# Kernel optimization log

Measured on AMD Instinct MI355X. Metric: run time of the kernel, lower is better.

The kernel has to match this reference:

```python
import jax, jax.numpy as jnp
import numpy as np

B, S, D, H = 4, 2048, 1024, 16
HD = D // H


def setup_inputs() -> dict:
    key = jax.random.key(0)
    k1, k2, k3 = jax.random.split(key, 3)
    x = jax.random.normal(k1, (B, S, D), dtype=jnp.float32)
    # xavier-ish scaling for stable softmax
    W_attn = jax.random.normal(k2, (3 * D, D), dtype=jnp.float32) * (1.0 / np.sqrt(2 * D))
    b_attn = jnp.zeros((3 * D,), dtype=jnp.float32)
    W_out = jax.random.normal(k3, (D, D), dtype=jnp.float32) * (1.0 / np.sqrt(D))
    b_out = jnp.zeros((D,), dtype=jnp.float32)
    return {"x": x, "W_attn": W_attn, "b_attn": b_attn, "W_out": W_out, "b_out": b_out}


def reference(x, W_attn, b_attn, W_out, b_out):
    bs, seq, d = x.shape
    # fused QKV projection (torch Linear: y = x @ W.T + b)
    kqv = jnp.einsum("bsd,ed->bse", x, W_attn) + b_attn
    # NOTE: source splits as k, q, v (k first)
    k, q, v = jnp.split(kqv, 3, axis=2)
    # [b, s, h, hd] -> [b, h, s, hd]
    k = k.reshape(bs, seq, H, HD).transpose(0, 2, 1, 3)
    q = q.reshape(bs, seq, H, HD).transpose(0, 2, 1, 3)
    v = v.reshape(bs, seq, H, HD).transpose(0, 2, 1, 3)
    scale = 1.0 / np.sqrt(HD)
    scores = jnp.einsum("bhqd,bhkd->bhqk", q, k) * scale
    attn = jax.nn.softmax(scores, axis=-1)
    y = jnp.einsum("bhqk,bhkd->bhqd", attn, v)
    y = y.transpose(0, 2, 1, 3).reshape(bs, seq, d)
    out = jnp.einsum("bsd,ed->bse", y, W_out) + b_out
    return out
```

## Files before the change

### kernel.cpp

```cpp
#include <hip/hip_runtime.h>

typedef unsigned short u16;
typedef unsigned int u32;
typedef __attribute__((ext_vector_type(2))) u32 u32x2;
typedef __attribute__((ext_vector_type(4))) u32 u32x4;
typedef __attribute__((ext_vector_type(8))) short bf16x8;
typedef __attribute__((ext_vector_type(4))) float f32x4;

__device__ __forceinline__ u16 f2bf(float f) {
  u32 b = __float_as_uint(f);
  b += 0x7fffu + ((b >> 16) & 1u);
  return (u16)(b >> 16);
}

__global__ __launch_bounds__(256) void cvt_f32_bf16(const float* __restrict__ in,
                                                    u16* __restrict__ out) {
  long i = ((long)blockIdx.x * 256 + threadIdx.x) * 8;
  u32 u[8];
#pragma unroll
  for (int j = 0; j < 8; j++) {
    u32 b = __float_as_uint(in[i + j]);
    u[j] = (b + 0x7fffu + ((b >> 16) & 1u)) >> 16;
  }
  u32x4 o;
  o[0] = u[0] | (u[1] << 16);
  o[1] = u[2] | (u[3] << 16);
  o[2] = u[4] | (u[5] << 16);
  o[3] = u[6] | (u[7] << 16);
  *(u32x4*)(out + i) = o;
}

#define LDST 72

__device__ __forceinline__ void gemm_core_128(const u16* __restrict__ A,
                                              const u16* __restrict__ B, int K,
                                              int m0, int n0, u16* As, u16* Bs,
                                              f32x4 acc[4][4]) {
  int t = threadIdx.x;
  int lane = t & 63, w = t >> 6;
  int quad = lane >> 4, l16 = lane & 15;
  int wm = (w >> 1) * 64, wn = (w & 1) * 64;
  int srow = t >> 3, sg = t & 7;
  for (int k0 = 0; k0 < K; k0 += 64) {
#pragma unroll
    for (int i = 0; i < 4; i++) {
      int row = i * 32 + srow;
      *(u32x4*)&As[row * LDST + sg * 8] =
          *(const u32x4*)&A[(long)(m0 + row) * K + k0 + sg * 8];
      *(u32x4*)&Bs[row * LDST + sg * 8] =
          *(const u32x4*)&B[(long)(n0 + row) * K + k0 + sg * 8];
    }
    __syncthreads();
#pragma unroll
    for (int ks = 0; ks < 2; ks++) {
      bf16x8 a[4], b[4];
#pragma unroll
      for (int tm = 0; tm < 4; tm++)
        a[tm] = *(const bf16x8*)&As[(wm + tm * 16 + l16) * LDST + ks * 32 + quad * 8];
#pragma unroll
      for (int tn = 0; tn < 4; tn++)
        b[tn] = *(const bf16x8*)&Bs[(wn + tn * 16 + l16) * LDST + ks * 32 + quad * 8];
#pragma unroll
      for (int tm = 0; tm < 4; tm++)
#pragma unroll
        for (int tn = 0; tn < 4; tn++)
          acc[tm][tn] = __builtin_amdgcn_mfma_f32_16x16x32_bf16(a[tm], b[tn],
                                                                acc[tm][tn], 0, 0, 0);
    }
    __syncthreads();
  }
}

__global__ __launch_bounds__(256) void gemm_qkv(const u16* __restrict__ A,
                                                const u16* __restrict__ B,
                                                const float* __restrict__ bias,
                                                u16* __restrict__ Kg,
                                                u16* __restrict__ Qg,
                                                u16* __restrict__ Vg) {
  __shared__ __align__(16) u16 As[128 * LDST];
  __shared__ __align__(16) u16 Bs[128 * LDST];
  const int K = 1024;
  int m0 = blockIdx.y * 128, n0 = blockIdx.x * 128;
  f32x4 acc[4][4];
#pragma unroll
  for (int i = 0; i < 4; i++)
#pragma unroll
    for (int j = 0; j < 4; j++) acc[i][j] = (f32x4)0.0f;
  gemm_core_128(A, B, K, m0, n0, As, Bs, acc);

  int t = threadIdx.x, lane = t & 63, w = t >> 6;
  int quad = lane >> 4, l16 = lane & 15;
  int wm = (w >> 1) * 64, wn = (w & 1) * 64;
#pragma unroll
  for (int tn = 0; tn < 4; tn++) {
    int n = n0 + wn + tn * 16 + l16;
    float bv = bias[n];
    int which = n >> 10;
    int h = (n >> 6) & 15, d = n & 63;
#pragma unroll
    for (int tm = 0; tm < 4; tm++) {
#pragma unroll
      for (int r = 0; r < 4; r++) {
        int m = m0 + wm + tm * 16 + quad * 4 + r;
        int b = m >> 11, s = m & 2047;
        float v = acc[tm][tn][r] + bv;
        long bh = (long)b * 16 + h;
        if (which == 0)
          Kg[(bh * 2048 + s) * 64 + d] = f2bf(v);
        else if (which == 1)
          Qg[(bh * 2048 + s) * 64 + d] = f2bf(v * 0.125f);
        else
          Vg[(bh * 64 + d) * 2048 + s] = f2bf(v);
      }
    }
  }
}

__global__ __launch_bounds__(256) void gemm_out(const u16* __restrict__ A,
                                                const u16* __restrict__ B,
                                                const float* __restrict__ bias,
                                                float* __restrict__ out) {
  __shared__ __align__(16) u16 As[128 * LDST];
  __shared__ __align__(16) u16 Bs[128 * LDST];
  const int K = 1024, N = 1024;
  int m0 = blockIdx.y * 128, n0 = blockIdx.x * 128;
  f32x4 acc[4][4];
#pragma unroll
  for (int i = 0; i < 4; i++)
#pragma unroll
    for (int j = 0; j < 4; j++) acc[i][j] = (f32x4)0.0f;
  gemm_core_128(A, B, K, m0, n0, As, Bs, acc);

  int t = threadIdx.x, lane = t & 63, w = t >> 6;
  int quad = lane >> 4, l16 = lane & 15;
  int wm = (w >> 1) * 64, wn = (w & 1) * 64;
#pragma unroll
  for (int tn = 0; tn < 4; tn++) {
    int n = n0 + wn + tn * 16 + l16;
    float bv = bias[n];
#pragma unroll
    for (int tm = 0; tm < 4; tm++) {
#pragma unroll
      for (int r = 0; r < 4; r++) {
        int m = m0 + wm + tm * 16 + quad * 4 + r;
        out[(long)m * N + n] = acc[tm][tn][r] + bv;
      }
    }
  }
}

__global__ __launch_bounds__(256, 4) void attn_kernel(const u16* __restrict__ Qg,
                                                      const u16* __restrict__ Kg,
                                                      const u16* __restrict__ Vg,
                                                      u16* __restrict__ Y) {
  __shared__ __align__(16) u16 Ks[64 * LDST];
  __shared__ __align__(16) u16 Vs[64 * LDST];
  __shared__ __align__(16) u16 Ps[4 * 32 * LDST];
  int t = threadIdx.x, lane = t & 63, w = t >> 6;
  int quad = lane >> 4, l16 = lane & 15;
  int bh = blockIdx.y;
  int q0 = blockIdx.x * 128 + w * 32;
  u16* Pw = Ps + w * 32 * LDST;

  bf16x8 qf[2][2];
#pragma unroll
  for (int tq = 0; tq < 2; tq++) {
    const u16* qp = Qg + ((long)bh * 2048 + q0 + tq * 16 + l16) * 64;
    qf[tq][0] = *(const bf16x8*)(qp + quad * 8);
    qf[tq][1] = *(const bf16x8*)(qp + 32 + quad * 8);
  }

  float lsum[2] = {0.0f, 0.0f};
  f32x4 acc[2][4];
#pragma unroll
  for (int tq = 0; tq < 2; tq++)
#pragma unroll
    for (int tn = 0; tn < 4; tn++) acc[tq][tn] = (f32x4)0.0f;

  int srow = t >> 3, sg = t & 7;
  for (int kv0 = 0; kv0 < 2048; kv0 += 64) {
#pragma unroll
    for (int i = 0; i < 2; i++) {
      int row = i * 32 + srow;
      *(u32x4*)&Ks[row * LDST + sg * 8] =
          *(const u32x4*)&Kg[((long)bh * 2048 + kv0 + row) * 64 + sg * 8];
      *(u32x4*)&Vs[row * LDST + sg * 8] =
          *(const u32x4*)&Vg[((long)bh * 64 + row) * 2048 + kv0 + sg * 8];
    }
    __syncthreads();

    f32x4 s[2][4];
#pragma unroll
    for (int tq = 0; tq < 2; tq++)
#pragma unroll
      for (int tn = 0; tn < 4; tn++) s[tq][tn] = (f32x4)0.0f;
#pragma unroll
    for (int ks = 0; ks < 2; ks++) {
      bf16x8 kf[4];
#pragma unroll
      for (int tn = 0; tn < 4; tn++)
        kf[tn] = *(const bf16x8*)&Ks[(tn * 16 + l16) * LDST + ks * 32 + quad * 8];
#pragma unroll
      for (int tq = 0; tq < 2; tq++)
#pragma unroll
        for (int tn = 0; tn < 4; tn++)
          s[tq][tn] = __builtin_amdgcn_mfma_f32_16x16x32_bf16(kf[tn], qf[tq][ks],
                                                              s[tq][tn], 0, 0, 0);
    }

#pragma unroll
    for (int tq = 0; tq < 2; tq++) {
#pragma unroll
      for (int tn = 0; tn < 4; tn++) {
        float e0 = __expf(s[tq][tn][0]);
        float e1 = __expf(s[tq][tn][1]);
        float e2 = __expf(s[tq][tn][2]);
        float e3 = __expf(s[tq][tn][3]);
        lsum[tq] += (e0 + e1) + (e2 + e3);
        u32x2 pk;
        pk[0] = (u32)f2bf(e0) | ((u32)f2bf(e1) << 16);
        pk[1] = (u32)f2bf(e2) | ((u32)f2bf(e3) << 16);
        *(u32x2*)&Pw[(tq * 16 + l16) * LDST + tn * 16 + quad * 4] = pk;
      }
    }

#pragma unroll
    for (int ks = 0; ks < 2; ks++) {
      bf16x8 vf[4];
#pragma unroll
      for (int tn = 0; tn < 4; tn++)
        vf[tn] = *(const bf16x8*)&Vs[(tn * 16 + l16) * LDST + ks * 32 + quad * 8];
#pragma unroll
      for (int tq = 0; tq < 2; tq++) {
        bf16x8 pf = *(const bf16x8*)&Pw[(tq * 16 + l16) * LDST + ks * 32 + quad * 8];
#pragma unroll
        for (int tn = 0; tn < 4; tn++)
          acc[tq][tn] = __builtin_amdgcn_mfma_f32_16x16x32_bf16(vf[tn], pf,
                                                                acc[tq][tn], 0, 0, 0);
      }
    }
    __syncthreads();
  }

#pragma unroll
  for (int tq = 0; tq < 2; tq++) {
    lsum[tq] += __shfl_xor(lsum[tq], 16, 64);
    lsum[tq] += __shfl_xor(lsum[tq], 32, 64);
  }

  int b = bh >> 4, h = bh & 15;
#pragma unroll
  for (int tq = 0; tq < 2; tq++) {
    float inv = 1.0f / lsum[tq];
    long row = (long)b * 2048 + q0 + tq * 16 + l16;
#pragma unroll
    for (int tn = 0; tn < 4; tn++) {
      u32x2 pk;
      pk[0] = (u32)f2bf(acc[tq][tn][0] * inv) | ((u32)f2bf(acc[tq][tn][1] * inv) << 16);
      pk[1] = (u32)f2bf(acc[tq][tn][2] * inv) | ((u32)f2bf(acc[tq][tn][3] * inv) << 16);
      *(u32x2*)&Y[row * 1024 + h * 64 + tn * 16 + quad * 4] = pk;
    }
  }
}

extern "C" void kernel_launch(void* const* d_in, const int* in_sizes, int n_in,
                              void* d_out, int out_size, void* d_ws, size_t ws_size,
                              hipStream_t stream) {
  const float* x = (const float*)d_in[0];
  const float* W_attn = (const float*)d_in[1];
  const float* b_attn = (const float*)d_in[2];
  const float* W_out = (const float*)d_in[3];
  const float* b_out = (const float*)d_in[4];
  float* out = (float*)d_out;

  char* ws = (char*)d_ws;
  u16* xb = (u16*)ws;
  u16* Wab = (u16*)(ws + 16777216);
  u16* Wob = (u16*)(ws + 16777216 + 6291456);
  u16* Kg = (u16*)(ws + 25165824);
  u16* Qg = Kg + 8388608;
  u16* Vg = Qg + 8388608;
  u16* Yb = xb;

  cvt_f32_bf16<<<4096, 256, 0, stream>>>(x, xb);
  cvt_f32_bf16<<<1536, 256, 0, stream>>>(W_attn, Wab);
  cvt_f32_bf16<<<512, 256, 0, stream>>>(W_out, Wob);

  gemm_qkv<<<dim3(24, 64), 256, 0, stream>>>(xb, Wab, b_attn, Kg, Qg, Vg);
  attn_kernel<<<dim3(16, 64), 256, 0, stream>>>(Qg, Kg, Vg, Yb);
  gemm_out<<<dim3(8, 64), 256, 0, stream>>>(Yb, Wob, b_out, out);
}
```

Measured before the change: 326.2 us.

## Use direct global-to-LDS loads with XOR swizzle, larger attention tiles, exp2 softmax

Replaces register-staged shared-memory fills with global_load_lds DMA and an XOR-swizzled unpadded LDS layout in both GEMMs and in attention. Attention now handles 64 query rows per wave, with K fragments held in registers and reused. Q is prescaled by log2(e)/8 so the hardware exp2 can be used, and bf16 packing uses the native convert. V stores in the QKV epilogue are vectorized. The aim is to cut LDS traffic, VALU conversion work and load instructions. The cost is higher register pressure and lower occupancy in attention.

```diff
diff --git a/kernel.cpp b/kernel.cpp
--- a/kernel.cpp
+++ b/kernel.cpp
@@ -13,6 +13,27 @@
   return (u16)(b >> 16);
 }
 
+__device__ __forceinline__ u32 pk2bf(float a, float b) {
+#if __has_builtin(__builtin_amdgcn_cvt_pk_bf16_f32)
+  return __builtin_bit_cast(u32, __builtin_amdgcn_cvt_pk_bf16_f32(a, b));
+#else
+  return (u32)f2bf(a) | ((u32)f2bf(b) << 16);
+#endif
+}
+
+__device__ __forceinline__ float fexp2(float x) {
+#if __has_builtin(__builtin_amdgcn_exp2f)
+  return __builtin_amdgcn_exp2f(x);
+#else
+  return exp2f(x);
+#endif
+}
+
+__device__ __forceinline__ void gload_lds16(const u16* g, u16* l) {
+  __builtin_amdgcn_global_load_lds((const __attribute__((address_space(1))) void*)g,
+                                   (__attribute__((address_space(3))) void*)l, 16, 0, 0);
+}
+
 __global__ __launch_bounds__(256) void cvt_f32_bf16(const float* __restrict__ in,
                                                     u16* __restrict__ out) {
   long i = ((long)blockIdx.x * 256 + threadIdx.x) * 8;
@@ -29,8 +50,6 @@
   o[3] = u[6] | (u[7] << 16);
   *(u32x4*)(out + i) = o;
 }
-
-#define LDST 72
 
 __device__ __forceinline__ void gemm_core_128(const u16* __restrict__ A,
                                               const u16* __restrict__ B, int K,
@@ -40,15 +59,15 @@
   int lane = t & 63, w = t >> 6;
   int quad = lane >> 4, l16 = lane & 15;
   int wm = (w >> 1) * 64, wn = (w & 1) * 64;
-  int srow = t >> 3, sg = t & 7;
+  int lr = lane >> 3, lc = lane & 7;
+  int cg = lc ^ lr;
+  int swz = l16 & 7;
   for (int k0 = 0; k0 < K; k0 += 64) {
 #pragma unroll
     for (int i = 0; i < 4; i++) {
-      int row = i * 32 + srow;
-      *(u32x4*)&As[row * LDST + sg * 8] =
-          *(const u32x4*)&A[(long)(m0 + row) * K + k0 + sg * 8];
-      *(u32x4*)&Bs[row * LDST + sg * 8] =
-          *(const u32x4*)&B[(long)(n0 + row) * K + k0 + sg * 8];
+      int r0 = i * 32 + w * 8;
+      gload_lds16(&A[(long)(m0 + r0 + lr) * K + k0 + cg * 8], &As[r0 * 64]);
+      gload_lds16(&B[(long)(n0 + r0 + lr) * K + k0 + cg * 8], &Bs[r0 * 64]);
     }
     __syncthreads();
 #pragma unroll
@@ -56,10 +75,10 @@
       bf16x8 a[4], b[4];
 #pragma unroll
       for (int tm = 0; tm < 4; tm++)
-        a[tm] = *(const bf16x8*)&As[(wm + tm * 16 + l16) * LDST + ks * 32 + quad * 8];
+        a[tm] = *(const bf16x8*)&As[(wm + tm * 16 + l16) * 64 + ((ks * 4 + quad) ^ swz) * 8];
 #pragma unroll
       for (int tn = 0; tn < 4; tn++)
-        b[tn] = *(const bf16x8*)&Bs[(wn + tn * 16 + l16) * LDST + ks * 32 + quad * 8];
+        b[tn] = *(const bf16x8*)&Bs[(wn + tn * 16 + l16) * 64 + ((ks * 4 + quad) ^ swz) * 8];
 #pragma unroll
       for (int tm = 0; tm < 4; tm++)
 #pragma unroll
@@ -71,14 +90,15 @@
   }
 }
 
+#define QSCALE 0.1803368801f
 __global__ __launch_bounds__(256) void gemm_qkv(const u16* __restrict__ A,
                                                 const u16* __restrict__ B,
                                                 const float* __restrict__ bias,
                                                 u16* __restrict__ Kg,
                                                 u16* __restrict__ Qg,
                                                 u16* __restrict__ Vg) {
-  __shared__ __align__(16) u16 As[128 * LDST];
-  __shared__ __align__(16) u16 Bs[128 * LDST];
+  __shared__ __align__(16) u16 As[128 * 64];
+  __shared__ __align__(16) u16 Bs[128 * 64];
   const int K = 1024;
   int m0 = blockIdx.y * 128, n0 = blockIdx.x * 128;
   f32x4 acc[4][4];
@@ -99,18 +119,23 @@
     int h = (n >> 6) & 15, d = n & 63;
 #pragma unroll
     for (int tm = 0; tm < 4; tm++) {
-#pragma unroll
-      for (int r = 0; r < 4; r++) {
-        int m = m0 + wm + tm * 16 + quad * 4 + r;
-        int b = m >> 11, s = m & 2047;
-        float v = acc[tm][tn][r] + bv;
-        long bh = (long)b * 16 + h;
-        if (which == 0)
-          Kg[(bh * 2048 + s) * 64 + d] = f2bf(v);
-        else if (which == 1)
-          Qg[(bh * 2048 + s) * 64 + d] = f2bf(v * 0.125f);
-        else
-          Vg[(bh * 64 + d) * 2048 + s] = f2bf(v);
+      int m = m0 + wm + tm * 16 + quad * 4;
+      int b = m >> 11, s = m & 2047;
+      long bh = (long)b * 16 + h;
+      if (which == 2) {
+        u32x2 pk;
+        pk[0] = pk2bf(acc[tm][tn][0] + bv, acc[tm][tn][1] + bv);
+        pk[1] = pk2bf(acc[tm][tn][2] + bv, acc[tm][tn][3] + bv);
+        *(u32x2*)&Vg[(bh * 64 + d) * 2048 + s] = pk;
+      } else {
+#pragma unroll
+        for (int r = 0; r < 4; r++) {
+          float v = acc[tm][tn][r] + bv;
+          if (which == 0)
+            Kg[(bh * 2048 + s + r) * 64 + d] = f2bf(v);
+          else
+            Qg[(bh * 2048 + s + r) * 64 + d] = f2bf(v * QSCALE);
+        }
       }
     }
   }
@@ -120,8 +145,8 @@
                                                 const u16* __restrict__ B,
                                                 const float* __restrict__ bias,
                                                 float* __restrict__ out) {
-  __shared__ __align__(16) u16 As[128 * LDST];
-  __shared__ __align__(16) u16 Bs[128 * LDST];
+  __shared__ __align__(16) u16 As[128 * 64];
+  __shared__ __align__(16) u16 Bs[128 * 64];
   const int K = 1024, N = 1024;
   int m0 = blockIdx.y * 128, n0 = blockIdx.x * 128;
   f32x4 acc[4][4];
@@ -149,78 +174,76 @@
   }
 }
 
-__global__ __launch_bounds__(256, 4) void attn_kernel(const u16* __restrict__ Qg,
+__global__ __launch_bounds__(256, 2) void attn_kernel(const u16* __restrict__ Qg,
                                                       const u16* __restrict__ Kg,
                                                       const u16* __restrict__ Vg,
                                                       u16* __restrict__ Y) {
-  __shared__ __align__(16) u16 Ks[64 * LDST];
-  __shared__ __align__(16) u16 Vs[64 * LDST];
-  __shared__ __align__(16) u16 Ps[4 * 32 * LDST];
+  __shared__ __align__(16) u16 Ks[64 * 64];
+  __shared__ __align__(16) u16 Vs[64 * 64];
+  __shared__ __align__(16) u16 Ps[4 * 64 * 64];
   int t = threadIdx.x, lane = t & 63, w = t >> 6;
   int quad = lane >> 4, l16 = lane & 15;
   int bh = blockIdx.y;
-  int q0 = blockIdx.x * 128 + w * 32;
-  u16* Pw = Ps + w * 32 * LDST;
-
-  bf16x8 qf[2][2];
-#pragma unroll
-  for (int tq = 0; tq < 2; tq++) {
+  int q0 = blockIdx.x * 256 + w * 64;
+  u16* Pw = Ps + w * 64 * 64;
+  int lr = lane >> 3, lc = lane & 7, cg = lc ^ lr;
+  int swz = l16 & 7;
+
+  bf16x8 qf[4][2];
+#pragma unroll
+  for (int tq = 0; tq < 4; tq++) {
     const u16* qp = Qg + ((long)bh * 2048 + q0 + tq * 16 + l16) * 64;
     qf[tq][0] = *(const bf16x8*)(qp + quad * 8);
     qf[tq][1] = *(const bf16x8*)(qp + 32 + quad * 8);
   }
 
-  float lsum[2] = {0.0f, 0.0f};
-  f32x4 acc[2][4];
-#pragma unroll
-  for (int tq = 0; tq < 2; tq++)
-#pragma unroll
-    for (int tn = 0; tn < 4; tn++) acc[tq][tn] = (f32x4)0.0f;
-
-  int srow = t >> 3, sg = t & 7;
+  float lsum[4] = {0.0f, 0.0f, 0.0f, 0.0f};
+  f32x4 acc[4][4];
+#pragma unroll
+  for (int tn = 0; tn < 4; tn++)
+#pragma unroll
+    for (int tq = 0; tq < 4; tq++) acc[tn][tq] = (f32x4)0.0f;
+
   for (int kv0 = 0; kv0 < 2048; kv0 += 64) {
 #pragma unroll
-    for (int i = 0; i < 2; i++) {
-      int row = i * 32 + srow;
-      *(u32x4*)&Ks[row * LDST + sg * 8] =
-          *(const u32x4*)&Kg[((long)bh * 2048 + kv0 + row) * 64 + sg * 8];
-      *(u32x4*)&Vs[row * LDST + sg * 8] =
-          *(const u32x4*)&Vg[((long)bh * 64 + row) * 2048 + kv0 + sg * 8];
+    for (int j = 0; j < 2; j++) {
+      int r0 = j * 32 + w * 8;
+      gload_lds16(&Kg[((long)bh * 2048 + kv0 + r0 + lr) * 64 + cg * 8], &Ks[r0 * 64]);
+      gload_lds16(&Vg[((long)bh * 64 + r0 + lr) * 2048 + kv0 + cg * 8], &Vs[r0 * 64]);
     }
     __syncthreads();
 
-    f32x4 s[2][4];
-#pragma unroll
-    for (int tq = 0; tq < 2; tq++)
-#pragma unroll
-      for (int tn = 0; tn < 4; tn++) s[tq][tn] = (f32x4)0.0f;
-#pragma unroll
-    for (int ks = 0; ks < 2; ks++) {
-      bf16x8 kf[4];
-#pragma unroll
-      for (int tn = 0; tn < 4; tn++)
-        kf[tn] = *(const bf16x8*)&Ks[(tn * 16 + l16) * LDST + ks * 32 + quad * 8];
-#pragma unroll
-      for (int tq = 0; tq < 2; tq++)
+    bf16x8 kf[4][2];
+#pragma unroll
+    for (int tn = 0; tn < 4; tn++)
+#pragma unroll
+      for (int ks = 0; ks < 2; ks++)
+        kf[tn][ks] = *(const bf16x8*)&Ks[(tn * 16 + l16) * 64 + ((ks * 4 + quad) ^ swz) * 8];
+
+#pragma unroll
+    for (int tq = 0; tq < 4; tq++) {
+      f32x4 s[4];
+#pragma unroll
+      for (int tn = 0; tn < 4; tn++) s[tn] = (f32x4)0.0f;
+#pragma unroll
+      for (int ks = 0; ks < 2; ks++)
 #pragma unroll
         for (int tn = 0; tn < 4; tn++)
-          s[tq][tn] = __builtin_amdgcn_mfma_f32_16x16x32_bf16(kf[tn], qf[tq][ks],
-                                                              s[tq][tn], 0, 0, 0);
-    }
-
-#pragma unroll
-    for (int tq = 0; tq < 2; tq++) {
+          s[tn] = __builtin_amdgcn_mfma_f32_16x16x32_bf16(kf[tn][ks], qf[tq][ks],
+                                                          s[tn], 0, 0, 0);
+      int qrow = tq * 16 + l16;
 #pragma unroll
       for (int tn = 0; tn < 4; tn++) {
-        float e0 = __expf(s[tq][tn][0]);
-        float e1 = __expf(s[tq][tn][1]);
-        float e2 = __expf(s[tq][tn][2]);
-        float e3 = __expf(s[tq][tn][3]);
+        float e0 = fexp2(s[tn][0]);
+        float e1 = fexp2(s[tn][1]);
+        float e2 = fexp2(s[tn][2]);
+        float e3 = fexp2(s[tn][3]);
         lsum[tq] += (e0 + e1) + (e2 + e3);
         u32x2 pk;
-        pk[0] = (u32)f2bf(e0) | ((u32)f2bf(e1) << 16);
-        pk[1] = (u32)f2bf(e2) | ((u32)f2bf(e3) << 16);
-        *(u32x2*)&Pw[(tq * 16 + l16) * LDST + tn * 16 + quad * 4] = pk;
+        pk[0] = pk2bf(e0, e1);
+        pk[1] = pk2bf(e2, e3);
+        int c2 = ((tn * 2 + (quad >> 1)) ^ swz) * 2 + (quad & 1);
+        *(u32x2*)&Pw[qrow * 64 + c2 * 4] = pk;
       }
     }
 
@@ -229,35 +252,35 @@
       bf16x8 vf[4];
 #pragma unroll
       for (int tn = 0; tn < 4; tn++)
-        vf[tn] = *(const bf16x8*)&Vs[(tn * 16 + l16) * LDST + ks * 32 + quad * 8];
-#pragma unroll
-      for (int tq = 0; tq < 2; tq++) {
-        bf16x8 pf = *(const bf16x8*)&Pw[(tq * 16 + l16) * LDST + ks * 32 + quad * 8];
+        vf[tn] = *(const bf16x8*)&Vs[(tn * 16 + l16) * 64 + ((ks * 4 + quad) ^ swz) * 8];
+#pragma unroll
+      for (int tq = 0; tq < 4; tq++) {
+        bf16x8 pf = *(const bf16x8*)&Pw[(tq * 16 + l16) * 64 + ((ks * 4 + quad) ^ swz) * 8];
 #pragma unroll
         for (int tn = 0; tn < 4; tn++)
-          acc[tq][tn] = __builtin_amdgcn_mfma_f32_16x16x32_bf16(vf[tn], pf,
-                                                                acc[tq][tn], 0, 0, 0);
+          acc[tn][tq] = __builtin_amdgcn_mfma_f32_16x16x32_bf16(vf[tn], pf,
+                                                                acc[tn][tq], 0, 0, 0);
       }
     }
     __syncthreads();
   }
 
 #pragma unroll
-  for (int tq = 0; tq < 2; tq++) {
+  for (int tq = 0; tq < 4; tq++) {
     lsum[tq] += __shfl_xor(lsum[tq], 16, 64);
     lsum[tq] += __shfl_xor(lsum[tq], 32, 64);
   }
 
   int b = bh >> 4, h = bh & 15;
 #pragma unroll
-  for (int tq = 0; tq < 2; tq++) {
+  for (int tq = 0; tq < 4; tq++) {
     float inv = 1.0f / lsum[tq];
     long row = (long)b * 2048 + q0 + tq * 16 + l16;
 #pragma unroll
     for (int tn = 0; tn < 4; tn++) {
       u32x2 pk;
-      pk[0] = (u32)f2bf(acc[tq][tn][0] * inv) | ((u32)f2bf(acc[tq][tn][1] * inv) << 16);
-      pk[1] = (u32)f2bf(acc[tq][tn][2] * inv) | ((u32)f2bf(acc[tq][tn][3] * inv) << 16);
+      pk[0] = pk2bf(acc[tn][tq][0] * inv, acc[tn][tq][1] * inv);
+      pk[1] = pk2bf(acc[tn][tq][2] * inv, acc[tn][tq][3] * inv);
       *(u32x2*)&Y[row * 1024 + h * 64 + tn * 16 + quad * 4] = pk;
     }
   }
@@ -287,6 +310,6 @@
   cvt_f32_bf16<<<512, 256, 0, stream>>>(W_out, Wob);
 
   gemm_qkv<<<dim3(24, 64), 256, 0, stream>>>(xb, Wab, b_attn, Kg, Qg, Vg);
-  attn_kernel<<<dim3(16, 64), 256, 0, stream>>>(Qg, Kg, Vg, Yb);
+  attn_kernel<<<dim3(8, 64), 256, 0, stream>>>(Qg, Kg, Vg, Yb);
   gemm_out<<<dim3(8, 64), 256, 0, stream>>>(Yb, Wob, b_out, out);
 }
```

New measurement: 286.4 us. -12.2%, faster.
